# Performance work log

Measured on AMD Instinct MI355X. Metric: run time of the kernel, lower is better.

Reference implementation:

```python
import jax, jax.numpy as jnp
import numpy as np

B, S, D, H = 4, 1024, 1024, 16
DK = D // H  # d_k = 64

def setup_inputs() -> dict:
    key = jax.random.key(0)
    ks = jax.random.split(key, 6)
    sc = 0.02
    return {
        "x": jax.random.normal(ks[0], (B, S, D), jnp.float32),
        "bias": jax.random.normal(ks[1], (H, S, S), jnp.float32),
        "Wq": jax.random.normal(ks[2], (D, D), jnp.float32) * sc,
        "Wk": jax.random.normal(ks[3], (D, D), jnp.float32) * sc,
        "Wv": jax.random.normal(ks[4], (D, D), jnp.float32) * sc,
        "Wo": jax.random.normal(ks[5], (D, D), jnp.float32) * sc,
    }

def _split_heads(t):
    # [B,S,D] -> [B,H,S,DK]
    b, s, _ = t.shape
    return t.reshape(b, s, H, DK).transpose(0, 2, 1, 3)

def reference(x, bias, Wq, Wk, Wv, Wo):
    q = _split_heads(x @ Wq)
    k = _split_heads(x @ Wk)
    v = _split_heads(x @ Wv)
    scale = jnp.asarray(DK, x.dtype) ** 0.5
    # [B,H,S,S] scores with additive per-head bias (broadcast over batch)
    attn = jnp.einsum('bhqd,bhkd->bhqk', q / scale, k) + bias[None]
    attn = jax.nn.softmax(attn, axis=-1)
    ctx = jnp.einsum('bhqk,bhkd->bhqd', attn, v)
    ctx = ctx.transpose(0, 2, 1, 3).reshape(x.shape[0], x.shape[1], -1)
    out = ctx @ Wo
    return (out, attn)
```

## Files before the change

kernel.cpp:

```cpp
#include <hip/hip_runtime.h>
#include <hip/hip_bf16.h>


typedef __bf16 bf16_t;
typedef __bf16 bf16x4 __attribute__((ext_vector_type(4)));
typedef __bf16 bf16x8 __attribute__((ext_vector_type(8)));
typedef float f32x4 __attribute__((ext_vector_type(4)));

#define MFMA16(a, b, c) __builtin_amdgcn_mfma_f32_16x16x32_bf16(a, b, c, 0, 0, 0)

__global__ __launch_bounds__(256) void prep(const float* __restrict__ x,
                                            const float* __restrict__ w0,
                                            const float* __restrict__ w1,
                                            const float* __restrict__ w2,
                                            const float* __restrict__ w3,
                                            bf16_t* __restrict__ xb,
                                            bf16_t* __restrict__ wt) {
    __shared__ float tile[32][33];
    const int tid = threadIdx.x;
    if (blockIdx.z == 4) {
        const int bid = blockIdx.y * 32 + blockIdx.x;
        const int base = bid * 1024 + tid;
#pragma unroll
        for (int k = 0; k < 4; ++k) {
            const int i = base + k * 256;
            float4 v = reinterpret_cast<const float4*>(x)[i];
            bf16x4 o = { (bf16_t)v.x, (bf16_t)v.y, (bf16_t)v.z, (bf16_t)v.w };
            reinterpret_cast<bf16x4*>(xb)[i] = o;
        }
        return;
    }
    const float* src = (blockIdx.z == 0) ? w0 : (blockIdx.z == 1) ? w1
                     : (blockIdx.z == 2) ? w2 : w3;
    bf16_t* dst = wt + (size_t)blockIdx.z * 1024 * 1024;
    const int r0 = blockIdx.y * 32, c0 = blockIdx.x * 32;
    const int tx = tid & 31, ty = tid >> 5;
#pragma unroll
    for (int k = 0; k < 4; ++k)
        tile[ty + k * 8][tx] = src[(size_t)(r0 + ty + k * 8) * 1024 + c0 + tx];
    __syncthreads();
#pragma unroll
    for (int k = 0; k < 4; ++k)
        dst[(size_t)(c0 + ty + k * 8) * 1024 + r0 + tx] = (bf16_t)tile[tx][ty + k * 8];
}

#define GEMM_BODY(A, BT)                                                                 \
    __shared__ bf16_t As[128 * 64];                                                      \
    __shared__ bf16_t Bs[128 * 64];                                                      \
    const int tid = threadIdx.x;                                                         \
    const int lane = tid & 63, wave = tid >> 6;                                          \
    const int lr = lane & 15, lg = lane >> 4;                                            \
    const int m_base = blockIdx.x * 128, n_base = blockIdx.y * 128;                      \
    const int wm = (wave >> 1) * 64, wn = (wave & 1) * 64;                               \
    int soff_[4];                                                                        \
    const bf16_t* aptr_[4];                                                              \
    const bf16_t* bptr_[4];                                                              \
    _Pragma("unroll") for (int i = 0; i < 4; ++i) {                                      \
        const int g = i * 256 + tid;                                                     \
        const int r = g >> 3, s = g & 7;                                                 \
        soff_[i] = r * 64 + ((s ^ (r & 7)) * 8);                                         \
        aptr_[i] = (A) + (size_t)(m_base + r) * 1024 + s * 8;                            \
        bptr_[i] = (BT) + (size_t)(n_base + r) * 1024 + s * 8;                           \
    }                                                                                    \
    bf16x8 ra_[4], rb_[4];                                                               \
    _Pragma("unroll") for (int i = 0; i < 4; ++i) {                                      \
        ra_[i] = *reinterpret_cast<const bf16x8*>(aptr_[i]);                             \
        rb_[i] = *reinterpret_cast<const bf16x8*>(bptr_[i]);                             \
    }                                                                                    \
    f32x4 acc[4][4] = {};                                                                \
    for (int kb = 64; kb <= 1024; kb += 64) {                                            \
        __syncthreads();                                                                 \
        _Pragma("unroll") for (int i = 0; i < 4; ++i) {                                  \
            *reinterpret_cast<bf16x8*>(&As[soff_[i]]) = ra_[i];                          \
            *reinterpret_cast<bf16x8*>(&Bs[soff_[i]]) = rb_[i];                          \
        }                                                                                \
        if (kb < 1024) {                                                                 \
            _Pragma("unroll") for (int i = 0; i < 4; ++i) {                              \
                ra_[i] = *reinterpret_cast<const bf16x8*>(aptr_[i] + kb);                \
                rb_[i] = *reinterpret_cast<const bf16x8*>(bptr_[i] + kb);                \
            }                                                                            \
        }                                                                                \
        __syncthreads();                                                                 \
        _Pragma("unroll") for (int h = 0; h < 2; ++h) {                                  \
            bf16x8 af[4], bfr[4];                                                        \
            _Pragma("unroll") for (int i = 0; i < 4; ++i) {                              \
                const int row = wm + i * 16 + lr;                                        \
                af[i] = *reinterpret_cast<const bf16x8*>(                                \
                    &As[row * 64 + (((h * 4 + lg) ^ (row & 7)) * 8)]);                   \
            }                                                                            \
            _Pragma("unroll") for (int j = 0; j < 4; ++j) {                              \
                const int row = wn + j * 16 + lr;                                        \
                bfr[j] = *reinterpret_cast<const bf16x8*>(                               \
                    &Bs[row * 64 + (((h * 4 + lg) ^ (row & 7)) * 8)]);                   \
            }                                                                            \
            _Pragma("unroll") for (int i = 0; i < 4; ++i)                                \
                _Pragma("unroll") for (int j = 0; j < 4; ++j)                            \
                    acc[i][j] = MFMA16(af[i], bfr[j], acc[i][j]);                        \
        }                                                                                \
    }

__global__ __launch_bounds__(256, 3) void gemm_qkv(const bf16_t* __restrict__ A,
                                                   const bf16_t* __restrict__ wT,
                                                   bf16_t* __restrict__ qhp,
                                                   bf16_t* __restrict__ khp,
                                                   bf16_t* __restrict__ vp) {
    const int z = blockIdx.z;
    const bf16_t* BT = wT + ((size_t)z << 20);
    GEMM_BODY(A, BT)
    bf16_t* dst = (z == 0) ? qhp : (z == 1) ? khp : vp;
    const float scale = (z == 0) ? 0.125f : 1.0f;
#pragma unroll
    for (int i = 0; i < 4; ++i)
#pragma unroll
        for (int j = 0; j < 4; ++j)
#pragma unroll
            for (int r = 0; r < 4; ++r) {
                const int row = m_base + wm + i * 16 + lg * 4 + r;
                const int col = n_base + wn + j * 16 + lr;
                const float v = acc[i][j][r] * scale;
                const int b = row >> 10, s = row & 1023;
                const int h = col >> 6, d = col & 63;
                const size_t bh16 = (size_t)(b * 16 + h) << 16;
                if (z == 2)
                    dst[bh16 + ((s >> 5) << 11) + d * 32 + (s & 31)] = (bf16_t)v;
                else
                    dst[bh16 + ((d >> 5) << 15) + s * 32 + (d & 31)] = (bf16_t)v;
            }
}

__global__ __launch_bounds__(256, 2) void gemm_out(const bf16_t* __restrict__ A,
                                                   const bf16_t* __restrict__ BT,
                                                   float* __restrict__ out) {
    __shared__ bf16_t As[64 * 64];
    __shared__ bf16_t Bs[128 * 64];
    const int tid = threadIdx.x;
    const int lane = tid & 63, wave = tid >> 6;
    const int lr = lane & 15, lg = lane >> 4;
    const int m_base = blockIdx.x * 64, n_base = blockIdx.y * 128;
    const int wm = (wave >> 1) * 32, wn = (wave & 1) * 64;

    int asoff[2];
    const bf16_t* aptr[2];
#pragma unroll
    for (int i = 0; i < 2; ++i) {
        const int g = i * 256 + tid;
        const int r = g >> 3, s = g & 7;
        asoff[i] = r * 64 + ((s ^ (r & 7)) * 8);
        aptr[i] = A + (size_t)(m_base + r) * 1024 + s * 8;
    }
    int bsoff[4];
    const bf16_t* bptr[4];
#pragma unroll
    for (int i = 0; i < 4; ++i) {
        const int g = i * 256 + tid;
        const int r = g >> 3, s = g & 7;
        bsoff[i] = r * 64 + ((s ^ (r & 7)) * 8);
        bptr[i] = BT + (size_t)(n_base + r) * 1024 + s * 8;
    }
    bf16x8 ra[2], rb[4];
#pragma unroll
    for (int i = 0; i < 2; ++i) ra[i] = *reinterpret_cast<const bf16x8*>(aptr[i]);
#pragma unroll
    for (int i = 0; i < 4; ++i) rb[i] = *reinterpret_cast<const bf16x8*>(bptr[i]);

    f32x4 acc[2][4] = {};
    for (int kb = 64; kb <= 1024; kb += 64) {
        __syncthreads();
#pragma unroll
        for (int i = 0; i < 2; ++i) *reinterpret_cast<bf16x8*>(&As[asoff[i]]) = ra[i];
#pragma unroll
        for (int i = 0; i < 4; ++i) *reinterpret_cast<bf16x8*>(&Bs[bsoff[i]]) = rb[i];
        if (kb < 1024) {
#pragma unroll
            for (int i = 0; i < 2; ++i) ra[i] = *reinterpret_cast<const bf16x8*>(aptr[i] + kb);
#pragma unroll
            for (int i = 0; i < 4; ++i) rb[i] = *reinterpret_cast<const bf16x8*>(bptr[i] + kb);
        }
        __syncthreads();
#pragma unroll
        for (int h = 0; h < 2; ++h) {
            bf16x8 af[2], bfr[4];
#pragma unroll
            for (int i = 0; i < 2; ++i) {
                const int row = wm + i * 16 + lr;
                af[i] = *reinterpret_cast<const bf16x8*>(
                    &As[row * 64 + (((h * 4 + lg) ^ (row & 7)) * 8)]);
            }
#pragma unroll
            for (int j = 0; j < 4; ++j) {
                const int row = wn + j * 16 + lr;
                bfr[j] = *reinterpret_cast<const bf16x8*>(
                    &Bs[row * 64 + (((h * 4 + lg) ^ (row & 7)) * 8)]);
            }
#pragma unroll
            for (int i = 0; i < 2; ++i)
#pragma unroll
                for (int j = 0; j < 4; ++j)
                    acc[i][j] = MFMA16(af[i], bfr[j], acc[i][j]);
        }
    }
#pragma unroll
    for (int i = 0; i < 2; ++i)
#pragma unroll
        for (int j = 0; j < 4; ++j)
#pragma unroll
            for (int r = 0; r < 4; ++r) {
                const int row = m_base + wm + i * 16 + lg * 4 + r;
                const int col = n_base + wn + j * 16 + lr;
                out[(size_t)row * 1024 + col] = acc[i][j][r];
            }
}

__global__ __launch_bounds__(256, 2) void fused_attn(const bf16_t* __restrict__ qhp,
                                                     const bf16_t* __restrict__ khp,
                                                     const bf16_t* __restrict__ vp,
                                                     const float* __restrict__ bias,
                                                     float* __restrict__ attn,
                                                     bf16_t* __restrict__ ctxb) {
    __shared__ f32x4 wlds4[4][1024];
    __shared__ float smaxp[128];
    __shared__ float ssump[128];
    const int lane = threadIdx.x & 63;
    const int wave = threadIdx.x >> 6;
    const int lr = lane & 15, lg = lane >> 4;

    const int g = blockIdx.x;
    const int j = g >> 3;
    const int h = (g & 7) + 8 * (j >> 7);
    const int qt = (j >> 2) & 31;
    const int b = j & 3;
    const int bh = b * 16 + h;
    const int m0 = qt * 32;

    const bf16_t* qbase = qhp + ((size_t)bh << 16);
    const bf16x8 aqA0 = *reinterpret_cast<const bf16x8*>(qbase + (m0 + lr) * 32 + lg * 8);
    const bf16x8 aqA1 = *reinterpret_cast<const bf16x8*>(qbase + 32768 + (m0 + lr) * 32 + lg * 8);
    const bf16x8 aqB0 = *reinterpret_cast<const bf16x8*>(qbase + (m0 + 16 + lr) * 32 + lg * 8);
    const bf16x8 aqB1 = *reinterpret_cast<const bf16x8*>(qbase + 32768 + (m0 + 16 + lr) * 32 + lg * 8);

    const int c0 = wave * 256;
    const bf16_t* kp0 = khp + ((size_t)bh << 16) + (size_t)(c0 + lr) * 32 + lg * 8;

    char* tw = reinterpret_cast<char*>(&wlds4[wave][0]);
    const int myswz = (lr & 7) << 4;

    const float* bb0 = bias + ((size_t)h << 20) + (size_t)m0 * 1024 + c0;
#pragma unroll
    for (int i = 0; i < 16; ++i) {
        const int co = (lane * 4) ^ ((i & 7) * 4);
        f32x4 bv = *reinterpret_cast<const f32x4*>(bb0 + (size_t)i * 1024 + co);
        *reinterpret_cast<f32x4*>(tw + i * 1024 + lane * 16) = bv;
    }
    f32x4 acc0[16];
#pragma unroll
    for (int f = 0; f < 16; ++f)
        acc0[f] = *reinterpret_cast<const f32x4*>(tw + lr * 1024 + ((f * 64 + lg * 16) ^ myswz));

    const float* bb1 = bb0 + 16 * 1024;
#pragma unroll
    for (int i = 0; i < 16; ++i) {
        const int co = (lane * 4) ^ ((i & 7) * 4);
        f32x4 bv = *reinterpret_cast<const f32x4*>(bb1 + (size_t)i * 1024 + co);
        *reinterpret_cast<f32x4*>(tw + i * 1024 + lane * 16) = bv;
    }
    f32x4 acc1[16];
#pragma unroll
    for (int f = 0; f < 16; ++f)
        acc1[f] = *reinterpret_cast<const f32x4*>(tw + lr * 1024 + ((f * 64 + lg * 16) ^ myswz));

#pragma unroll
    for (int half = 0; half < 2; ++half) {
        const bf16x8 aqA = half ? aqA1 : aqA0;
        const bf16x8 aqB = half ? aqB1 : aqB0;
#pragma unroll
        for (int bt = 0; bt < 2; ++bt) {
            bf16x8 kf[8];
#pragma unroll
            for (int u = 0; u < 8; ++u)
                kf[u] = *reinterpret_cast<const bf16x8*>(
                    kp0 + half * 32768 + (bt * 8 + u) * 512);
#pragma unroll
            for (int u = 0; u < 8; ++u) {
                acc0[bt * 8 + u] = MFMA16(kf[u], aqA, acc0[bt * 8 + u]);
                acc1[bt * 8 + u] = MFMA16(kf[u], aqB, acc1[bt * 8 + u]);
            }
        }
    }

    f32x4 m40 = acc0[0], m41 = acc1[0];
#pragma unroll
    for (int f = 1; f < 16; ++f) {
#pragma unroll
        for (int r = 0; r < 4; ++r) {
            m40[r] = fmaxf(m40[r], acc0[f][r]);
            m41[r] = fmaxf(m41[r], acc1[f][r]);
        }
    }
    float mx0 = fmaxf(fmaxf(m40[0], m40[1]), fmaxf(m40[2], m40[3]));
    float mx1 = fmaxf(fmaxf(m41[0], m41[1]), fmaxf(m41[2], m41[3]));
    mx0 = fmaxf(mx0, __shfl_xor(mx0, 16));
    mx0 = fmaxf(mx0, __shfl_xor(mx0, 32));
    mx1 = fmaxf(mx1, __shfl_xor(mx1, 16));
    mx1 = fmaxf(mx1, __shfl_xor(mx1, 32));
    if (lane < 16) {
        smaxp[wave * 16 + lr] = mx0;
        smaxp[64 + wave * 16 + lr] = mx1;
    }
    __syncthreads();
    const float gm0 = fmaxf(fmaxf(smaxp[lr], smaxp[16 + lr]),
                            fmaxf(smaxp[32 + lr], smaxp[48 + lr]));
    const float gm1 = fmaxf(fmaxf(smaxp[64 + lr], smaxp[80 + lr]),
                            fmaxf(smaxp[96 + lr], smaxp[112 + lr]));

    f32x4 s40 = {0.f, 0.f, 0.f, 0.f}, s41 = {0.f, 0.f, 0.f, 0.f};
#pragma unroll
    for (int f = 0; f < 16; ++f) {
#pragma unroll
        for (int r = 0; r < 4; ++r) {
            const float e0 = __expf(acc0[f][r] - gm0);
            const float e1 = __expf(acc1[f][r] - gm1);
            acc0[f][r] = e0;
            acc1[f][r] = e1;
            s40[r] += e0;
            s41[r] += e1;
        }
    }
    float sm0 = (s40[0] + s40[1]) + (s40[2] + s40[3]);
    float sm1 = (s41[0] + s41[1]) + (s41[2] + s41[3]);
    sm0 += __shfl_xor(sm0, 16);
    sm0 += __shfl_xor(sm0, 32);
    sm1 += __shfl_xor(sm1, 16);
    sm1 += __shfl_xor(sm1, 32);
    if (lane < 16) {
        ssump[wave * 16 + lr] = sm0;
        ssump[64 + wave * 16 + lr] = sm1;
    }
    __syncthreads();
    const float invl0 = 1.0f / (ssump[lr] + ssump[16 + lr] + ssump[32 + lr] + ssump[48 + lr]);
    const float invl1 = 1.0f / (ssump[64 + lr] + ssump[80 + lr] + ssump[96 + lr] + ssump[112 + lr]);

    const bf16_t* vpb = vp + ((size_t)bh << 16) + (size_t)(wave * 8) * 2048 + lr * 32 + lg * 8;
    bf16x8 vf0[4][4];
#pragma unroll
    for (int ks = 0; ks < 4; ++ks)
#pragma unroll
        for (int f2 = 0; f2 < 4; ++f2)
            vf0[ks][f2] = *reinterpret_cast<const bf16x8*>(vpb + ks * 2048 + f2 * 512);

#pragma unroll
    for (int f = 0; f < 16; ++f) {
        f32x4 v0 = acc0[f], v1 = acc1[f];
#pragma unroll
        for (int r = 0; r < 4; ++r) { v0[r] *= invl0; v1[r] *= invl1; }
        bf16x4 p0 = { (bf16_t)v0[0], (bf16_t)v0[1], (bf16_t)v0[2], (bf16_t)v0[3] };
        bf16x4 p1 = { (bf16_t)v1[0], (bf16_t)v1[1], (bf16_t)v1[2], (bf16_t)v1[3] };
        const int ro = lr * 512 + ((f * 32 + lg * 8) ^ myswz);
        *reinterpret_cast<bf16x4*>(tw + ro) = p0;
        *reinterpret_cast<bf16x4*>(tw + 8192 + ro) = p1;
    }

    {
        float* obase = attn + ((size_t)bh << 20) + (size_t)m0 * 1024 + c0;
#pragma unroll
        for (int i = 0; i < 16; ++i) {
            const int cc = (lane * 4) ^ ((i & 7) * 8);
            bf16x4 q0 = *reinterpret_cast<const bf16x4*>(tw + i * 512 + lane * 8);
            bf16x4 q1 = *reinterpret_cast<const bf16x4*>(tw + 8192 + i * 512 + lane * 8);
            f32x4 w0 = { (float)q0[0], (float)q0[1], (float)q0[2], (float)q0[3] };
            f32x4 w1 = { (float)q1[0], (float)q1[1], (float)q1[2], (float)q1[3] };
            *reinterpret_cast<f32x4*>(obase + (size_t)i * 1024 + cc) = w0;
            *reinterpret_cast<f32x4*>(obase + (size_t)(16 + i) * 1024 + cc) = w1;
        }
    }

    f32x4 cacc0[4], cacc1[4];
#pragma unroll
    for (int f2 = 0; f2 < 4; ++f2) {
        cacc0[f2] = (f32x4){0.f, 0.f, 0.f, 0.f};
        cacc1[f2] = (f32x4){0.f, 0.f, 0.f, 0.f};
    }
    bf16x8 vf1[4][4];
#pragma unroll
    for (int ks = 0; ks < 4; ++ks)
#pragma unroll
        for (int f2 = 0; f2 < 4; ++f2)
            vf1[ks][f2] = *reinterpret_cast<const bf16x8*>(vpb + (4 + ks) * 2048 + f2 * 512);

#pragma unroll
    for (int ks = 0; ks < 4; ++ks) {
        const int po = lr * 512 + ((ks * 64 + lg * 16) ^ myswz);
        bf16x8 pa0 = *reinterpret_cast<const bf16x8*>(tw + po);
        bf16x8 pa1 = *reinterpret_cast<const bf16x8*>(tw + 8192 + po);
#pragma unroll
        for (int f2 = 0; f2 < 4; ++f2) {
            cacc0[f2] = MFMA16(pa0, vf0[ks][f2], cacc0[f2]);
            cacc1[f2] = MFMA16(pa1, vf0[ks][f2], cacc1[f2]);
        }
    }
#pragma unroll
    for (int ks = 4; ks < 8; ++ks) {
        const int po = lr * 512 + ((ks * 64 + lg * 16) ^ myswz);
        bf16x8 pa0 = *reinterpret_cast<const bf16x8*>(tw + po);
        bf16x8 pa1 = *reinterpret_cast<const bf16x8*>(tw + 8192 + po);
#pragma unroll
        for (int f2 = 0; f2 < 4; ++f2) {
            cacc0[f2] = MFMA16(pa0, vf1[ks - 4][f2], cacc0[f2]);
            cacc1[f2] = MFMA16(pa1, vf1[ks - 4][f2], cacc1[f2]);
        }
    }

    {
        float* credw = reinterpret_cast<float*>(tw);
#pragma unroll
        for (int f2 = 0; f2 < 4; ++f2)
#pragma unroll
            for (int r = 0; r < 4; ++r) {
                credw[(lg * 4 + r) * 64 + f2 * 16 + lr] = cacc0[f2][r];
                credw[1024 + (lg * 4 + r) * 64 + f2 * 16 + lr] = cacc1[f2][r];
            }
    }
    __syncthreads();
    const int row_l = wave * 4 + lg;
    const int dk0 = lr * 4;
#pragma unroll
    for (int t = 0; t < 2; ++t) {
        f32x4 s0 = *reinterpret_cast<const f32x4*>(
            reinterpret_cast<const float*>(&wlds4[0][0]) + t * 1024 + row_l * 64 + dk0);
        f32x4 s1 = *reinterpret_cast<const f32x4*>(
            reinterpret_cast<const float*>(&wlds4[1][0]) + t * 1024 + row_l * 64 + dk0);
        f32x4 s2 = *reinterpret_cast<const f32x4*>(
            reinterpret_cast<const float*>(&wlds4[2][0]) + t * 1024 + row_l * 64 + dk0);
        f32x4 s3 = *reinterpret_cast<const f32x4*>(
            reinterpret_cast<const float*>(&wlds4[3][0]) + t * 1024 + row_l * 64 + dk0);
        f32x4 st = (s0 + s1) + (s2 + s3);
        bf16x4 o4 = { (bf16_t)st[0], (bf16_t)st[1], (bf16_t)st[2], (bf16_t)st[3] };
        *reinterpret_cast<bf16x4*>(
            &ctxb[(size_t)(b * 1024 + m0 + t * 16 + row_l) * 1024 + h * 64 + dk0]) = o4;
    }
}

extern "C" void kernel_launch(void* const* d_in, const int* in_sizes, int n_in,
                              void* d_out, int out_size, void* d_ws, size_t ws_size,
                              hipStream_t stream) {
    const float* x    = (const float*)d_in[0];
    const float* bias = (const float*)d_in[1];
    const float* Wq   = (const float*)d_in[2];
    const float* Wk   = (const float*)d_in[3];
    const float* Wv   = (const float*)d_in[4];
    const float* Wo   = (const float*)d_in[5];
    float* out  = (float*)d_out;
    float* attn = out + (size_t)4 * 1024 * 1024;

    char* ws = (char*)d_ws;
    bf16_t* xb   = (bf16_t*)(ws);
    bf16_t* wT   = (bf16_t*)(ws + ((size_t)8 << 20));
    bf16_t* qhp  = (bf16_t*)(ws + ((size_t)16 << 20));
    bf16_t* khp  = (bf16_t*)(ws + ((size_t)24 << 20));
    bf16_t* vp   = (bf16_t*)(ws + ((size_t)32 << 20));
    bf16_t* ctxb = (bf16_t*)(ws + ((size_t)40 << 20));
    bf16_t* woT = wT + ((size_t)3 << 20);

    prep<<<dim3(32, 32, 5), dim3(256), 0, stream>>>(x, Wq, Wk, Wv, Wo, xb, wT);

    gemm_qkv<<<dim3(32, 8, 3), dim3(256), 0, stream>>>(xb, wT, qhp, khp, vp);

    fused_attn<<<dim3(2048), dim3(256), 0, stream>>>(qhp, khp, vp, bias, attn, ctxb);

    gemm_out<<<dim3(64, 8), dim3(256), 0, stream>>>(ctxb, woT, out);
}
```

Measured before the change: 170.9 us.

## Double-buffer LDS tiles in QKV and output GEMMs to halve barriers

Both GEMM kernels now keep two LDS buffers for the A and B tiles. Each iteration writes the next k-tile into the spare buffer while computing on the current one, so only one __syncthreads per iteration is needed instead of two. This doubles LDS use per block (64 KB in gemm_qkv), and the launch bound for gemm_qkv drops from 3 to 2 blocks per CU, which may lower occupancy.

```diff
diff --git a/kernel.cpp b/kernel.cpp
--- a/kernel.cpp
+++ b/kernel.cpp
@@ -45,8 +45,8 @@
 }
 
 #define GEMM_BODY(A, BT)                                                                 \
-    __shared__ bf16_t As[128 * 64];                                                      \
-    __shared__ bf16_t Bs[128 * 64];                                                      \
+    __shared__ bf16_t As[2][128 * 64];                                                   \
+    __shared__ bf16_t Bs[2][128 * 64];                                                   \
     const int tid = threadIdx.x;                                                         \
     const int lane = tid & 63, wave = tid >> 6;                                          \
     const int lr = lane & 15, lg = lane >> 4;                                            \
@@ -67,39 +67,51 @@
         ra_[i] = *reinterpret_cast<const bf16x8*>(aptr_[i]);                             \
         rb_[i] = *reinterpret_cast<const bf16x8*>(bptr_[i]);                             \
     }                                                                                    \
+    _Pragma("unroll") for (int i = 0; i < 4; ++i) {                                      \
+        *reinterpret_cast<bf16x8*>(&As[0][soff_[i]]) = ra_[i];                           \
+        *reinterpret_cast<bf16x8*>(&Bs[0][soff_[i]]) = rb_[i];                           \
+    }                                                                                    \
+    _Pragma("unroll") for (int i = 0; i < 4; ++i) {                                      \
+        ra_[i] = *reinterpret_cast<const bf16x8*>(aptr_[i] + 64);                        \
+        rb_[i] = *reinterpret_cast<const bf16x8*>(bptr_[i] + 64);                        \
+    }                                                                                    \
+    __syncthreads();                                                                     \
     f32x4 acc[4][4] = {};                                                                \
-    for (int kb = 64; kb <= 1024; kb += 64) {                                            \
-        __syncthreads();                                                                 \
-        _Pragma("unroll") for (int i = 0; i < 4; ++i) {                                  \
-            *reinterpret_cast<bf16x8*>(&As[soff_[i]]) = ra_[i];                          \
-            *reinterpret_cast<bf16x8*>(&Bs[soff_[i]]) = rb_[i];                          \
+    for (int t = 0; t < 16; ++t) {                                                       \
+        const int cur = t & 1, nxt = cur ^ 1;                                            \
+        if (t < 15) {                                                                    \
+            _Pragma("unroll") for (int i = 0; i < 4; ++i) {                              \
+                *reinterpret_cast<bf16x8*>(&As[nxt][soff_[i]]) = ra_[i];                 \
+                *reinterpret_cast<bf16x8*>(&Bs[nxt][soff_[i]]) = rb_[i];                 \
+            }                                                                            \
         }                                                                                \
-        if (kb < 1024) {                                                                 \
+        if (t < 14) {                                                                    \
+            const int kb = (t + 2) * 64;                                                 \
             _Pragma("unroll") for (int i = 0; i < 4; ++i) {                              \
                 ra_[i] = *reinterpret_cast<const bf16x8*>(aptr_[i] + kb);                \
                 rb_[i] = *reinterpret_cast<const bf16x8*>(bptr_[i] + kb);                \
             }                                                                            \
         }                                                                                \
-        __syncthreads();                                                                 \
         _Pragma("unroll") for (int h = 0; h < 2; ++h) {                                  \
             bf16x8 af[4], bfr[4];                                                        \
             _Pragma("unroll") for (int i = 0; i < 4; ++i) {                              \
                 const int row = wm + i * 16 + lr;                                        \
                 af[i] = *reinterpret_cast<const bf16x8*>(                                \
-                    &As[row * 64 + (((h * 4 + lg) ^ (row & 7)) * 8)]);                   \
+                    &As[cur][row * 64 + (((h * 4 + lg) ^ (row & 7)) * 8)]);              \
             }                                                                            \
             _Pragma("unroll") for (int j = 0; j < 4; ++j) {                              \
                 const int row = wn + j * 16 + lr;                                        \
                 bfr[j] = *reinterpret_cast<const bf16x8*>(                               \
-                    &Bs[row * 64 + (((h * 4 + lg) ^ (row & 7)) * 8)]);                   \
+                    &Bs[cur][row * 64 + (((h * 4 + lg) ^ (row & 7)) * 8)]);              \
             }                                                                            \
             _Pragma("unroll") for (int i = 0; i < 4; ++i)                                \
                 _Pragma("unroll") for (int j = 0; j < 4; ++j)                            \
                     acc[i][j] = MFMA16(af[i], bfr[j], acc[i][j]);                        \
         }                                                                                \
-    }
-
-__global__ __launch_bounds__(256, 3) void gemm_qkv(const bf16_t* __restrict__ A,
+        __syncthreads();                                                                 \
+    }
+
+__global__ __launch_bounds__(256, 2) void gemm_qkv(const bf16_t* __restrict__ A,
                                                    const bf16_t* __restrict__ wT,
                                                    bf16_t* __restrict__ qhp,
                                                    bf16_t* __restrict__ khp,
@@ -131,8 +143,8 @@
 __global__ __launch_bounds__(256, 2) void gemm_out(const bf16_t* __restrict__ A,
                                                    const bf16_t* __restrict__ BT,
                                                    float* __restrict__ out) {
-    __shared__ bf16_t As[64 * 64];
-    __shared__ bf16_t Bs[128 * 64];
+    __shared__ bf16_t As[2][64 * 64];
+    __shared__ bf16_t Bs[2][128 * 64];
     const int tid = threadIdx.x;
     const int lane = tid & 63, wave = tid >> 6;
     const int lr = lane & 15, lg = lane >> 4;
@@ -162,21 +174,32 @@
     for (int i = 0; i < 2; ++i) ra[i] = *reinterpret_cast<const bf16x8*>(aptr[i]);
 #pragma unroll
     for (int i = 0; i < 4; ++i) rb[i] = *reinterpret_cast<const bf16x8*>(bptr[i]);
+#pragma unroll
+    for (int i = 0; i < 2; ++i) *reinterpret_cast<bf16x8*>(&As[0][asoff[i]]) = ra[i];
+#pragma unroll
+    for (int i = 0; i < 4; ++i) *reinterpret_cast<bf16x8*>(&Bs[0][bsoff[i]]) = rb[i];
+#pragma unroll
+    for (int i = 0; i < 2; ++i) ra[i] = *reinterpret_cast<const bf16x8*>(aptr[i] + 64);
+#pragma unroll
+    for (int i = 0; i < 4; ++i) rb[i] = *reinterpret_cast<const bf16x8*>(bptr[i] + 64);
+    __syncthreads();
 
     f32x4 acc[2][4] = {};
-    for (int kb = 64; kb <= 1024; kb += 64) {
-        __syncthreads();
-#pragma unroll
-        for (int i = 0; i < 2; ++i) *reinterpret_cast<bf16x8*>(&As[asoff[i]]) = ra[i];
-#pragma unroll
-        for (int i = 0; i < 4; ++i) *reinterpret_cast<bf16x8*>(&Bs[bsoff[i]]) = rb[i];
-        if (kb < 1024) {
+    for (int t = 0; t < 16; ++t) {
+        const int cur = t & 1, nxt = cur ^ 1;
+        if (t < 15) {
+#pragma unroll
+            for (int i = 0; i < 2; ++i) *reinterpret_cast<bf16x8*>(&As[nxt][asoff[i]]) = ra[i];
+#pragma unroll
+            for (int i = 0; i < 4; ++i) *reinterpret_cast<bf16x8*>(&Bs[nxt][bsoff[i]]) = rb[i];
+        }
+        if (t < 14) {
+            const int kb = (t + 2) * 64;
 #pragma unroll
             for (int i = 0; i < 2; ++i) ra[i] = *reinterpret_cast<const bf16x8*>(aptr[i] + kb);
 #pragma unroll
             for (int i = 0; i < 4; ++i) rb[i] = *reinterpret_cast<const bf16x8*>(bptr[i] + kb);
         }
-        __syncthreads();
 #pragma unroll
         for (int h = 0; h < 2; ++h) {
             bf16x8 af[2], bfr[4];
@@ -184,13 +207,13 @@
             for (int i = 0; i < 2; ++i) {
                 const int row = wm + i * 16 + lr;
                 af[i] = *reinterpret_cast<const bf16x8*>(
-                    &As[row * 64 + (((h * 4 + lg) ^ (row & 7)) * 8)]);
+                    &As[cur][row * 64 + (((h * 4 + lg) ^ (row & 7)) * 8)]);
             }
 #pragma unroll
             for (int j = 0; j < 4; ++j) {
                 const int row = wn + j * 16 + lr;
                 bfr[j] = *reinterpret_cast<const bf16x8*>(
-                    &Bs[row * 64 + (((h * 4 + lg) ^ (row & 7)) * 8)]);
+                    &Bs[cur][row * 64 + (((h * 4 + lg) ^ (row & 7)) * 8)]);
             }
 #pragma unroll
             for (int i = 0; i < 2; ++i)
@@ -198,6 +221,7 @@
                 for (int j = 0; j < 4; ++j)
                     acc[i][j] = MFMA16(af[i], bfr[j], acc[i][j]);
         }
+        __syncthreads();
     }
 #pragma unroll
     for (int i = 0; i < 2; ++i)
```

Measured after the change: 171.6 us. About the same (+0.4%).
